# Kernel tuning notes

Hardware: AMD Instinct MI355X
Metric: run time of the kernel (lower is better)

## Reference

```python
import jax, jax.numpy as jnp
import numpy as np
from jax import lax

B, T, H, C = 1024, 128, 256, 10


def setup_inputs() -> dict:
    key = jax.random.key(0)
    ks = jax.random.split(key, 16)
    inp = {
        "x": jax.random.normal(ks[0], (B, T), dtype=jnp.float32),
        # torch.randn-initialized input weights (input_dim=1)
        "w_gx": jax.random.normal(ks[1], (1, H), dtype=jnp.float32),
        "w_ix": jax.random.normal(ks[2], (1, H), dtype=jnp.float32),
        "w_fx": jax.random.normal(ks[3], (1, H), dtype=jnp.float32),
        "w_ox": jax.random.normal(ks[4], (1, H), dtype=jnp.float32),
        # torch.rand-initialized recurrent weights
        "w_gh": jax.random.uniform(ks[5], (H, H), dtype=jnp.float32),
        "w_ih": jax.random.uniform(ks[6], (H, H), dtype=jnp.float32),
        "w_fh": jax.random.uniform(ks[7], (H, H), dtype=jnp.float32),
        "w_oh": jax.random.uniform(ks[8], (H, H), dtype=jnp.float32),
        "b_g": jax.random.uniform(ks[9], (H,), dtype=jnp.float32),
        "b_i": jax.random.uniform(ks[10], (H,), dtype=jnp.float32),
        "b_f": jax.random.uniform(ks[11], (H,), dtype=jnp.float32),
        "b_o": jax.random.uniform(ks[12], (H,), dtype=jnp.float32),
        "w_ph": jax.random.normal(ks[13], (H, C), dtype=jnp.float32),
        "b_p": jax.random.uniform(ks[14], (C,), dtype=jnp.float32),
    }
    return inp


def reference(x, w_gx, w_ix, w_fx, w_ox, w_gh, w_ih, w_fh, w_oh,
              b_g, b_i, b_f, b_o, w_ph, b_p):
    # Fuse the 4 gate projections into one GEMM per step (same math, order: g,i,f,o)
    Wx = jnp.concatenate([w_gx, w_ix, w_fx, w_ox], axis=1)   # (1, 4H)
    Wh = jnp.concatenate([w_gh, w_ih, w_fh, w_oh], axis=1)   # (H, 4H)
    b = jnp.concatenate([b_g, b_i, b_f, b_o])                 # (4H,)
    h0 = jnp.zeros((x.shape[0], w_gh.shape[0]), dtype=x.dtype)
    c0 = jnp.zeros_like(h0)

    def step(carry, xt):
        h, c = carry
        # xt: (B,) scalar input per example -> (B,1) @ (1,4H)
        z = xt[:, None] @ Wx + h @ Wh + b                     # (B, 4H)
        g, i, f, o = jnp.split(z, 4, axis=1)
        g = jnp.tanh(g)
        i = jax.nn.sigmoid(i)
        f = jax.nn.sigmoid(f)
        o = jax.nn.sigmoid(o)
        c = g * i + c * f
        h = jnp.tanh(c) * o
        return (h, c), None

    (h, _), _ = lax.scan(step, (h0, c0), x.T)                  # scan over time (T, B)
    return h @ w_ph + b_p                                      # (B, num_classes)
```

## Files before the change

### kernel.cpp

```cpp
#include <hip/hip_runtime.h>


#define TSTEPS  128
#define HDIM    256
#define NCLS    10
#define BB      4
#define NBLOCKS 256
#define NTHR    1024

#define XSTR    132
#define HSTR    320
#define PSTR    260

typedef char  i8x16 __attribute__((ext_vector_type(16)));
typedef int   i32x4 __attribute__((ext_vector_type(4)));

#define L2E     1.4426950408889634f
#define MGC     (-2.0f * L2E)
#define SMG     (-2.0f * L2E / 16129.0f)
#define SMS     (-1.0f * L2E / 16129.0f)

static __device__ __forceinline__ float rcpf(float x) { return __builtin_amdgcn_rcpf(x); }
static __device__ __forceinline__ float exp2f_fast(float x) { return __builtin_amdgcn_exp2f(x); }

#define MFMA_I8(ACC, A, B) \
    asm("v_mfma_i32_16x16x64_i8 %0, %1, %2, %0" : "+v"(ACC) : "v"(A), "a"(B))

#define EXTRACT(V) (s1 ? (s0 ? (V)[3] : (V)[2]) : (s0 ? (V)[1] : (V)[0]))

static __device__ __forceinline__ float gate_h(float zs0, float zs1, float zs2,
                                               float zs3, float& c)
{
    const float eg = exp2f_fast(zs0), ei = exp2f_fast(zs1);
    const float ef = exp2f_fast(zs2), eo = exp2f_fast(zs3);
    const float rg = rcpf(1.0f + eg), ri = rcpf(1.0f + ei);
    const float rf = rcpf(1.0f + ef), ro = rcpf(1.0f + eo);
    const float gg = __builtin_fmaf(2.0f, rg, -1.0f);
    const float cc = __builtin_fmaf(c, rf, gg * ri);
    c = cc;
    const float et = exp2f_fast(cc * MGC);
    const float rt = rcpf(1.0f + et);
    const float tc = __builtin_fmaf(2.0f, rt, -1.0f);
    return tc * ro;
}

__global__ __launch_bounds__(64)
void pack_w(const float* __restrict__ wg, const float* __restrict__ wi,
            const float* __restrict__ wf, const float* __restrict__ wo,
            signed char* __restrict__ wq8)
{
    const int b = blockIdx.x;
    const int q = b >> 8;
    const int u = b & 255;
    const float* wp = (q == 0) ? wg : (q == 1) ? wi : (q == 2) ? wf : wo;
    const int t  = threadIdx.x;
    const int k0 = t * 4;
    unsigned int pk = 0;
#pragma unroll
    for (int i = 0; i < 4; ++i) {
        const float v = wp[(k0 + i) * HDIM + u];
        int qv = __float2int_rn(v * 127.0f);
        qv = (qv > 127) ? 127 : ((qv < -127) ? -127 : qv);
        pk |= ((unsigned int)qv & 255u) << (8 * i);
    }
    *(unsigned int*)(wq8 + ((size_t)(q * 256 + u) * 256 + k0)) = pk;
}

__global__ __launch_bounds__(NTHR, 4)
void lstm_full(const float* __restrict__ x,
               const float* __restrict__ w_gx, const float* __restrict__ w_ix,
               const float* __restrict__ w_fx, const float* __restrict__ w_ox,
               const float* __restrict__ b_g,  const float* __restrict__ b_i,
               const float* __restrict__ b_f,  const float* __restrict__ b_o,
               const float* __restrict__ w_ph, const float* __restrict__ b_p,
               const signed char* __restrict__ wq8,
               float* __restrict__ out)
{
    const int g    = blockIdx.x;
    const int tid  = threadIdx.x;
    const int w    = tid >> 6;
    const int lane = tid & 63;
    const int l16  = lane & 15;
    const int lq   = lane >> 4;

    __shared__ float        x_lds[BB * XSTR];
    __shared__ signed char  h_q[2][BB * HSTR];
    __shared__ float        proj[BB * PSTR];

    {
        const float* xs = x + (size_t)g * BB * TSTEPS;
        for (int i = tid; i < BB * TSTEPS; i += NTHR)
            x_lds[(i >> 7) * XSTR + (i & 127)] = xs[i];
    }

    const int u = w * 16 + l16;
    i32x4 wa[4][4];
#pragma unroll
    for (int q = 0; q < 4; ++q)
#pragma unroll
        for (int kk = 0; kk < 4; ++kk) {
            const signed char* p = wq8 + ((size_t)(q * 256 + u) * 256)
                                       + kk * 64 + lq * 16;
            i32x4 v = __builtin_bit_cast(i32x4, *(const i8x16*)p);
            asm volatile("" : "+a"(v));
            wa[q][kk] = v;
        }

    const float* const wxp[4] = {w_gx, w_ix, w_fx, w_ox};
    const float* const bbp[4] = {b_g, b_i, b_f, b_o};
    float wxm[4], bm[4];
#pragma unroll
    for (int q = 0; q < 4; ++q) {
        const float m = (q == 0) ? MGC : (-L2E);
        wxm[q] = wxp[q][u] * m;
        bm[q]  = bbp[q][u] * m;
    }

    float c = 0.f;
    const bool s0 = (lq & 1) != 0;
    const bool s1 = (lq & 2) != 0;
    const int  woff = lq * HSTR + u;

    __syncthreads();

    {
        const float xv = x_lds[lq * XSTR + 0];
        const float hh = gate_h(__builtin_fmaf(xv, wxm[0], bm[0]),
                                __builtin_fmaf(xv, wxm[1], bm[1]),
                                __builtin_fmaf(xv, wxm[2], bm[2]),
                                __builtin_fmaf(xv, wxm[3], bm[3]), c);
        h_q[1][woff] = (signed char)__float2int_rn(hh * 127.0f);
        __syncthreads();
    }

    for (int t = 1; t < TSTEPS; ++t) {
        const signed char* hs = &h_q[t & 1][(l16 & 3) * HSTR];
        const i32x4 ah0 = *(const i32x4*)(hs +   0 + lq * 16);
        const i32x4 ah1 = *(const i32x4*)(hs +  64 + lq * 16);
        const i32x4 ah2 = *(const i32x4*)(hs + 128 + lq * 16);
        const i32x4 ah3 = *(const i32x4*)(hs + 192 + lq * 16);

        i32x4 a[4] = {{0,0,0,0},{0,0,0,0},{0,0,0,0},{0,0,0,0}};
#pragma unroll
        for (int q = 0; q < 4; ++q) MFMA_I8(a[q], ah0, wa[q][0]);
#pragma unroll
        for (int q = 0; q < 4; ++q) MFMA_I8(a[q], ah1, wa[q][1]);
#pragma unroll
        for (int q = 0; q < 4; ++q) MFMA_I8(a[q], ah2, wa[q][2]);
#pragma unroll
        for (int q = 0; q < 4; ++q) MFMA_I8(a[q], ah3, wa[q][3]);

        const float xv = x_lds[lq * XSTR + t];
        const float zs0 = __builtin_fmaf((float)EXTRACT(a[0]), SMG,
                          __builtin_fmaf(xv, wxm[0], bm[0]));
        const float zs1 = __builtin_fmaf((float)EXTRACT(a[1]), SMS,
                          __builtin_fmaf(xv, wxm[1], bm[1]));
        const float zs2 = __builtin_fmaf((float)EXTRACT(a[2]), SMS,
                          __builtin_fmaf(xv, wxm[2], bm[2]));
        const float zs3 = __builtin_fmaf((float)EXTRACT(a[3]), SMS,
                          __builtin_fmaf(xv, wxm[3], bm[3]));
        const float hh = gate_h(zs0, zs1, zs2, zs3, c);

        h_q[(t + 1) & 1][woff] = (signed char)__float2int_rn(hh * 127.0f);
        if (t == TSTEPS - 1) proj[lq * PSTR + u] = hh;
        __syncthreads();
    }

    if (tid < BB * NCLS) {
        const int r = tid / NCLS, cls = tid - r * NCLS;
        float a = b_p[cls];
#pragma unroll 8
        for (int uu = 0; uu < HDIM; ++uu)
            a = __builtin_fmaf(proj[r * PSTR + uu], w_ph[uu * NCLS + cls], a);
        out[(size_t)(g * BB + r) * NCLS + cls] = a;
    }
}

extern "C" void kernel_launch(void* const* d_in, const int* in_sizes, int n_in,
                              void* d_out, int out_size, void* d_ws, size_t ws_size,
                              hipStream_t stream)
{
    const float* x    = (const float*)d_in[0];
    const float* w_gx = (const float*)d_in[1];
    const float* w_ix = (const float*)d_in[2];
    const float* w_fx = (const float*)d_in[3];
    const float* w_ox = (const float*)d_in[4];
    const float* w_gh = (const float*)d_in[5];
    const float* w_ih = (const float*)d_in[6];
    const float* w_fh = (const float*)d_in[7];
    const float* w_oh = (const float*)d_in[8];
    const float* b_g  = (const float*)d_in[9];
    const float* b_i  = (const float*)d_in[10];
    const float* b_f  = (const float*)d_in[11];
    const float* b_o  = (const float*)d_in[12];
    const float* w_ph = (const float*)d_in[13];
    const float* b_p  = (const float*)d_in[14];

    signed char* wq8 = (signed char*)d_ws;

    hipLaunchKernelGGL(pack_w, dim3(1024), dim3(64), 0, stream,
                       w_gh, w_ih, w_fh, w_oh, wq8);

    hipLaunchKernelGGL(lstm_full, dim3(NBLOCKS), dim3(NTHR), 0, stream,
                       x, w_gx, w_ix, w_fx, w_ox,
                       b_g, b_i, b_f, b_o, w_ph, b_p,
                       wq8, (float*)d_out);
}
```

Measured before the change: 124.6 us.

## Replace per-step workgroup barriers with per-wave LDS flags and triple-buffered hidden state

The per-timestep __syncthreads is replaced by per-wave release/acquire flags in LDS. Each wave publishes its step counter after writing its slice of quantized h. Consumers spin only on the flags of the waves whose 64-wide K chunk they are about to feed into the MFMA, so slow waves no longer stall everyone at a full barrier. The hidden-state buffer becomes triple-buffered so a wave running one step ahead cannot overwrite data still being read. The cost is spin-polling LDS traffic and reliance on wave-level memory ordering of the release store.

Measured after the change: 137.2 us. 1.1x slower.

```diff
diff --git a/kernel.cpp b/kernel.cpp
--- a/kernel.cpp
+++ b/kernel.cpp
@@ -10,6 +10,7 @@
 
 #define XSTR    132
 #define HSTR    320
+#define HBUF    (BB * HSTR)
 #define PSTR    260
 
 typedef char  i8x16 __attribute__((ext_vector_type(16)));
@@ -84,14 +85,16 @@
     const int lq   = lane >> 4;
 
     __shared__ float        x_lds[BB * XSTR];
-    __shared__ signed char  h_q[2][BB * HSTR];
+    __shared__ signed char  h_q[3 * HBUF];
     __shared__ float        proj[BB * PSTR];
+    __shared__ int          flg[16];
 
     {
         const float* xs = x + (size_t)g * BB * TSTEPS;
         for (int i = tid; i < BB * TSTEPS; i += NTHR)
             x_lds[(i >> 7) * XSTR + (i & 127)] = xs[i];
     }
+    if (tid < 16) flg[tid] = 0;
 
     const int u = w * 16 + l16;
     i32x4 wa[4][4];
@@ -120,6 +123,7 @@
     const bool s0 = (lq & 1) != 0;
     const bool s1 = (lq & 2) != 0;
     const int  woff = lq * HSTR + u;
+    const int  fi   = lane & 3;
 
     __syncthreads();
 
@@ -129,26 +133,27 @@
                                 __builtin_fmaf(xv, wxm[1], bm[1]),
                                 __builtin_fmaf(xv, wxm[2], bm[2]),
                                 __builtin_fmaf(xv, wxm[3], bm[3]), c);
-        h_q[1][woff] = (signed char)__float2int_rn(hh * 127.0f);
-        __syncthreads();
-    }
+        h_q[HBUF + woff] = (signed char)__float2int_rn(hh * 127.0f);
+        if (lane == 0)
+            __hip_atomic_store(&flg[w], 1, __ATOMIC_RELEASE,
+                               __HIP_MEMORY_SCOPE_WORKGROUP);
+    }
+
+    int oR = HBUF, oW = 2 * HBUF, oS = 0;
 
     for (int t = 1; t < TSTEPS; ++t) {
-        const signed char* hs = &h_q[t & 1][(l16 & 3) * HSTR];
-        const i32x4 ah0 = *(const i32x4*)(hs +   0 + lq * 16);
-        const i32x4 ah1 = *(const i32x4*)(hs +  64 + lq * 16);
-        const i32x4 ah2 = *(const i32x4*)(hs + 128 + lq * 16);
-        const i32x4 ah3 = *(const i32x4*)(hs + 192 + lq * 16);
-
+        const signed char* hs = &h_q[oR + (l16 & 3) * HSTR];
         i32x4 a[4] = {{0,0,0,0},{0,0,0,0},{0,0,0,0},{0,0,0,0}};
-#pragma unroll
-        for (int q = 0; q < 4; ++q) MFMA_I8(a[q], ah0, wa[q][0]);
-#pragma unroll
-        for (int q = 0; q < 4; ++q) MFMA_I8(a[q], ah1, wa[q][1]);
-#pragma unroll
-        for (int q = 0; q < 4; ++q) MFMA_I8(a[q], ah2, wa[q][2]);
-#pragma unroll
-        for (int q = 0; q < 4; ++q) MFMA_I8(a[q], ah3, wa[q][3]);
+
+#pragma unroll
+        for (int kk = 0; kk < 4; ++kk) {
+            while (__hip_atomic_load(&flg[4 * kk + fi], __ATOMIC_ACQUIRE,
+                                     __HIP_MEMORY_SCOPE_WORKGROUP) < t) { }
+            const i32x4 ah = *(const i32x4*)(hs + kk * 64 + lq * 16);
+#pragma unroll
+            for (int q = 0; q < 4; ++q)
+                MFMA_I8(a[q], ah, wa[q][kk]);
+        }
 
         const float xv = x_lds[lq * XSTR + t];
         const float zs0 = __builtin_fmaf((float)EXTRACT(a[0]), SMG,
@@ -161,10 +166,17 @@
                           __builtin_fmaf(xv, wxm[3], bm[3]));
         const float hh = gate_h(zs0, zs1, zs2, zs3, c);
 
-        h_q[(t + 1) & 1][woff] = (signed char)__float2int_rn(hh * 127.0f);
+        h_q[oW + woff] = (signed char)__float2int_rn(hh * 127.0f);
         if (t == TSTEPS - 1) proj[lq * PSTR + u] = hh;
-        __syncthreads();
-    }
+
+        if (lane == 0)
+            __hip_atomic_store(&flg[w], t + 1, __ATOMIC_RELEASE,
+                               __HIP_MEMORY_SCOPE_WORKGROUP);
+
+        const int tmp = oS; oS = oR; oR = oW; oW = tmp;
+    }
+
+    __syncthreads();
 
     if (tid < BB * NCLS) {
         const int r = tid / NCLS, cls = tid - r * NCLS;
```
